# Kernel optimization log

Measured on AMD Instinct MI355X. Metric: run time of the kernel, lower is better.

Reference implementation:

```python
import jax, jax.numpy as jnp
import numpy as np

B, T, E, H = 2, 2048, 1024, 16
HS = E // H  # head size 64


def setup_inputs() -> dict:
    key = jax.random.key(0)
    ks = jax.random.split(key, 6)
    s = 0.02
    return {
        "x": jax.random.normal(ks[0], (B, T, E), dtype=jnp.float32),
        "Wq": jax.random.normal(ks[1], (E, E), dtype=jnp.float32) * s,
        "Wk": jax.random.normal(ks[2], (E, E), dtype=jnp.float32) * s,
        "Wv": jax.random.normal(ks[3], (E, E), dtype=jnp.float32) * s,
        "Wp": jax.random.normal(ks[4], (E, E), dtype=jnp.float32) * s,
        "bp": jax.random.normal(ks[5], (E,), dtype=jnp.float32) * s,
    }


def reference(x, Wq, Wk, Wv, Wp, bp):
    b, t, e = x.shape
    # per-head projections (concatenated heads == single E->E matmul, reshaped)
    def heads(w):
        return jnp.einsum('bte,ef->btf', x, w).reshape(b, t, H, HS).transpose(0, 2, 1, 3)
    q, k, v = heads(Wq), heads(Wk), heads(Wv)  # [B,H,T,HS]
    # NOTE: original scales by full embed dim E, not head_size
    scores = jnp.einsum('bhqd,bhkd->bhqk', q, k) * (e ** -0.5)
    causal = jnp.tril(jnp.ones((t, t), dtype=bool))
    scores = jnp.where(causal, scores, -jnp.inf)
    probs = jax.nn.softmax(scores, axis=-1)
    # dropout is identity in eval mode
    out = jnp.einsum('bhqk,bhkd->bhqd', probs, v)  # [B,H,T,HS]
    out = out.transpose(0, 2, 1, 3).reshape(b, t, e)
    return jnp.einsum('bte,ef->btf', out, Wp) + bp
```

## Files before the change

kernel.cpp:

```cpp
#include <hip/hip_runtime.h>
#include <math.h>

typedef __bf16 bf16x8 __attribute__((ext_vector_type(8)));
typedef __bf16 bf16x4 __attribute__((ext_vector_type(4)));
typedef float f32x4 __attribute__((ext_vector_type(4)));

constexpr int Bb = 2, Tt = 2048, Ee = 1024, Hh = 16, Hs = 64;
constexpr int Mm = Bb * Tt;

__device__ inline unsigned short f2bf(float f) {
    union { float f; unsigned u; } c; c.f = f;
    unsigned u = c.u;
    u += 0x7FFFu + ((u >> 16) & 1u);
    return (unsigned short)(u >> 16);
}

__device__ inline void gl2lds16(const void* g, void* l) {
    __builtin_amdgcn_global_load_lds(
        (const __attribute__((address_space(1))) void*)g,
        (__attribute__((address_space(3))) void*)l, 16, 0, 0);
}

__global__ __launch_bounds__(256) void prep(const float* __restrict__ x,
                                            const float* __restrict__ Wq,
                                            const float* __restrict__ Wk,
                                            const float* __restrict__ Wv,
                                            const float* __restrict__ Wp,
                                            unsigned short* __restrict__ xb,
                                            unsigned short* __restrict__ wt3,
                                            unsigned short* __restrict__ wpt) {
    const int tid = threadIdx.x;
    if (blockIdx.z == 4) {
        int flat = (blockIdx.y * 16 + blockIdx.x) * 256 + tid;
#pragma unroll
        for (int i = 0; i < 16; i++) {
            int gid = flat + i * 65536;
            float4 v = ((const float4*)x)[gid];
            ushort4 o;
            o.x = f2bf(v.x); o.y = f2bf(v.y); o.z = f2bf(v.z); o.w = f2bf(v.w);
            ((ushort4*)xb)[gid] = o;
        }
        return;
    }
    __shared__ unsigned short t[64][68];
    const float* W = (blockIdx.z == 0) ? Wq : (blockIdx.z == 1) ? Wk
                    : (blockIdx.z == 2) ? Wv : Wp;
    unsigned short* dst = (blockIdx.z < 3) ? wt3 + (size_t)blockIdx.z * 1024 * 1024 : wpt;
    const int k0 = blockIdx.x * 64, n0 = blockIdx.y * 64;
#pragma unroll
    for (int j = 0; j < 4; j++) {
        int row = (tid >> 4) + j * 16;
        int c4 = (tid & 15) * 4;
        float4 v = *(const float4*)&W[(size_t)(k0 + row) * 1024 + n0 + c4];
        t[row][c4 + 0] = f2bf(v.x); t[row][c4 + 1] = f2bf(v.y);
        t[row][c4 + 2] = f2bf(v.z); t[row][c4 + 3] = f2bf(v.w);
    }
    __syncthreads();
#pragma unroll
    for (int j = 0; j < 16; j++) {
        int flat = j * 256 + tid;
        int orow = flat >> 6, ocol = flat & 63;
        dst[(size_t)(n0 + orow) * 1024 + k0 + ocol] = t[ocol][orow];
    }
}

__device__ inline void gemm_mainloop(const unsigned short* __restrict__ A,
                                     const unsigned short* __restrict__ Bt,
                                     unsigned short* As, unsigned short* Bs,
                                     int bm, int bn, int tid, f32x4 (&acc)[4][4]) {
    const int lane = tid & 63, w = tid >> 6;
    const int quad = lane >> 4, cl = lane & 15;
    const int wm = (w >> 1) * 64, wn = (w & 1) * 64;

    auto stage = [&](int k0) {
#pragma unroll
        for (int i = 0; i < 2; i++) {
            int L = tid + i * 256;
            int r = L >> 2;
            int kc = (L & 3) ^ (r & 3);
            gl2lds16(A + (size_t)(bm + r) * 1024 + k0 + kc * 8, &As[L * 8]);
        }
#pragma unroll
        for (int i = 0; i < 2; i++) {
            int L = tid + i * 256;
            int r = L >> 2;
            int kc = (L & 3) ^ (r & 3);
            gl2lds16(Bt + (size_t)(bn + r) * 1024 + k0 + kc * 8, &Bs[L * 8]);
        }
    };

    stage(0);
    __syncthreads();
    for (int k0 = 0;;) {
        bf16x8 af[4], bfr[4];
#pragma unroll
        for (int mt = 0; mt < 4; mt++) {
            int r = wm + mt * 16 + cl;
            af[mt] = *(const bf16x8*)&As[(r * 4 + (quad ^ (r & 3))) * 8];
            int rb = wn + mt * 16 + cl;
            bfr[mt] = *(const bf16x8*)&Bs[(rb * 4 + (quad ^ (rb & 3))) * 8];
        }
#pragma unroll
        for (int mt = 0; mt < 4; mt++)
#pragma unroll
            for (int nt = 0; nt < 4; nt++)
                acc[mt][nt] = __builtin_amdgcn_mfma_f32_16x16x32_bf16(
                    af[mt], bfr[nt], acc[mt][nt], 0, 0, 0);
        k0 += 32;
        if (k0 >= 1024) break;
        __syncthreads();
        stage(k0);
        __syncthreads();
    }
}

__global__ __launch_bounds__(256, 2) void gemm_qkv(const unsigned short* __restrict__ A,
                                                   const unsigned short* __restrict__ Bt,
                                                   unsigned short* __restrict__ qb,
                                                   unsigned short* __restrict__ kb,
                                                   unsigned short* __restrict__ vtb) {
    __shared__ unsigned short As[128 * 32];
    __shared__ unsigned short Bs[128 * 32];
    const int tid = threadIdx.x;
    const int bm = blockIdx.y * 128;
    const int bn = blockIdx.x * 128;
    f32x4 acc[4][4] = {};
    gemm_mainloop(A, Bt, As, Bs, bm, bn, tid, acc);

    const int lane = tid & 63, w = tid >> 6;
    const int quad = lane >> 4, cl = lane & 15;
    const int wm = (w >> 1) * 64, wn = (w & 1) * 64;
    const int region = bn >> 10;

    if (region < 2) {
        unsigned short* dst = region ? kb : qb;
        const float qs = region ? 1.0f : 0.045084220027780107f;
#pragma unroll
        for (int mt = 0; mt < 4; mt++)
#pragma unroll
            for (int nt = 0; nt < 4; nt++)
#pragma unroll
                for (int rg = 0; rg < 4; rg++) {
                    int m = bm + wm + mt * 16 + quad * 4 + rg;
                    int nn = (bn + wn + nt * 16 + cl) & 1023;
                    int b = m >> 11, t = m & 2047, h = nn >> 6, hs = nn & 63;
                    dst[((size_t)(b * 16 + h) * 2048 + t) * 64 + hs] =
                        f2bf(acc[mt][nt][rg] * qs);
                }
    } else {
#pragma unroll
        for (int mt = 0; mt < 4; mt++) {
            int m0 = bm + wm + mt * 16 + quad * 4;
            int b = m0 >> 11, t0 = m0 & 2047;
#pragma unroll
            for (int nt = 0; nt < 4; nt++) {
                int nn = (bn + wn + nt * 16 + cl) & 1023;
                int h = nn >> 6, hs = nn & 63;
                ushort4 pk;
                pk.x = f2bf(acc[mt][nt][0]); pk.y = f2bf(acc[mt][nt][1]);
                pk.z = f2bf(acc[mt][nt][2]); pk.w = f2bf(acc[mt][nt][3]);
                *(ushort4*)&vtb[((size_t)(b * 16 + h) * 64 + hs) * 2048 + t0] = pk;
            }
        }
    }
}

__global__ __launch_bounds__(256, 4) void gemm_out(const unsigned short* __restrict__ A,
                                                   const unsigned short* __restrict__ Bt,
                                                   const float* __restrict__ bias,
                                                   float* __restrict__ out) {
    __shared__ unsigned short As[64 * 32];
    __shared__ unsigned short Bs[128 * 32];
    const int tid = threadIdx.x;
    const int bm = blockIdx.y * 64;
    const int bn = blockIdx.x * 128;
    const int lane = tid & 63, w = tid >> 6;
    const int quad = lane >> 4, cl = lane & 15;
    const int wm = (w >> 1) * 32, wn = (w & 1) * 64;
    f32x4 acc[2][4] = {};

    auto stage = [&](int k0) {
        {
            int L = tid;
            int r = L >> 2;
            int kc = (L & 3) ^ (r & 3);
            gl2lds16(A + (size_t)(bm + r) * 1024 + k0 + kc * 8, &As[L * 8]);
        }
#pragma unroll
        for (int i = 0; i < 2; i++) {
            int L = tid + i * 256;
            int r = L >> 2;
            int kc = (L & 3) ^ (r & 3);
            gl2lds16(Bt + (size_t)(bn + r) * 1024 + k0 + kc * 8, &Bs[L * 8]);
        }
    };

    stage(0);
    __syncthreads();
    for (int k0 = 0;;) {
        bf16x8 af[2], bfr[4];
#pragma unroll
        for (int mt = 0; mt < 2; mt++) {
            int r = wm + mt * 16 + cl;
            af[mt] = *(const bf16x8*)&As[(r * 4 + (quad ^ (r & 3))) * 8];
        }
#pragma unroll
        for (int nt = 0; nt < 4; nt++) {
            int rb = wn + nt * 16 + cl;
            bfr[nt] = *(const bf16x8*)&Bs[(rb * 4 + (quad ^ (rb & 3))) * 8];
        }
#pragma unroll
        for (int mt = 0; mt < 2; mt++)
#pragma unroll
            for (int nt = 0; nt < 4; nt++)
                acc[mt][nt] = __builtin_amdgcn_mfma_f32_16x16x32_bf16(
                    af[mt], bfr[nt], acc[mt][nt], 0, 0, 0);
        k0 += 32;
        if (k0 >= 1024) break;
        __syncthreads();
        stage(k0);
        __syncthreads();
    }

#pragma unroll
    for (int mt = 0; mt < 2; mt++)
#pragma unroll
        for (int nt = 0; nt < 4; nt++)
#pragma unroll
            for (int rg = 0; rg < 4; rg++) {
                int m = bm + wm + mt * 16 + quad * 4 + rg;
                int n = bn + wn + nt * 16 + cl;
                out[(size_t)m * 1024 + n] = acc[mt][nt][rg] + bias[n];
            }
}

__global__ __launch_bounds__(256, 3) void attn_mfma(const unsigned short* __restrict__ qg,
                                                    const unsigned short* __restrict__ kg,
                                                    const unsigned short* __restrict__ vtg,
                                                    unsigned short* __restrict__ og) {
    __shared__ unsigned short Qlds[128 * 64];
    __shared__ unsigned short Klds[2][64 * 64];
    __shared__ unsigned short Vlds[2][64 * 64];
    const int tid = threadIdx.x;
    const int idx = blockIdx.x;
    const int bh = idx & 31;
    const int j = 15 - (idx >> 5);
    const int lane = tid & 63, w = tid >> 6;
    const int quad = lane >> 4, cl = lane & 15;
    const int qbase = j * 128;
    const int wq0 = w * 32;
    const unsigned short* qB = qg + (size_t)bh * 2048 * 64;
    const unsigned short* kB = kg + (size_t)bh * 2048 * 64;
    const unsigned short* vB = vtg + (size_t)bh * 64 * 2048;

    auto stageKV = [&](int kt, int buf) {
#pragma unroll
        for (int i = 0; i < 2; i++) {
            int L = tid + i * 256;
            int r = L >> 3;
            int kc = (L & 7) ^ (r & 7);
            gl2lds16(kB + (size_t)(kt * 64 + r) * 64 + kc * 8, &Klds[buf][L * 8]);
            gl2lds16(vB + (size_t)r * 2048 + kt * 64 + kc * 8, &Vlds[buf][L * 8]);
        }
    };

#pragma unroll
    for (int i = 0; i < 4; i++) {
        int L = tid + i * 256;
        int r = L >> 3;
        int kc = (L & 7) ^ (r & 7);
        gl2lds16(qB + (size_t)(qbase + r) * 64 + kc * 8, &Qlds[L * 8]);
    }
    stageKV(0, 0);
    __syncthreads();

    bf16x8 qf[2][2];
#pragma unroll
    for (int nt2 = 0; nt2 < 2; nt2++)
#pragma unroll
        for (int kf = 0; kf < 2; kf++) {
            int r = wq0 + nt2 * 16 + cl, cc = kf * 4 + quad;
            qf[nt2][kf] = *(const bf16x8*)&Qlds[(r * 8 + (cc ^ (r & 7))) * 8];
        }

    bf16x8 ones;
#pragma unroll
    for (int i = 0; i < 8; i++) ones[i] = (__bf16)1.0f;

    f32x4 oacc[2][4] = {};
    f32x4 lacc[2] = {};
    unsigned short* Pw = &Qlds[w * 2048];
    const int ntiles = 2 * j + 2;
    const int dkt = 2 * j + (w >> 1);
    const int qloc0 = (w & 1) * 32;

    for (int kt = 0; kt < ntiles; kt++) {
        const int buf = kt & 1;
        if (kt + 1 < ntiles) stageKV(kt + 1, buf ^ 1);
        if (kt <= dkt) {
            const bool diag = (kt == dkt);
            f32x4 sac[4][2] = {};
#pragma unroll
            for (int kf = 0; kf < 2; kf++)
#pragma unroll
                for (int mt = 0; mt < 4; mt++) {
                    int r = mt * 16 + cl, cc = kf * 4 + quad;
                    bf16x8 kf8 = *(const bf16x8*)&Klds[buf][(r * 8 + (cc ^ (r & 7))) * 8];
#pragma unroll
                    for (int nt2 = 0; nt2 < 2; nt2++)
                        sac[mt][nt2] = __builtin_amdgcn_mfma_f32_16x16x32_bf16(
                            kf8, qf[nt2][kf], sac[mt][nt2], 0, 0, 0);
                }
#pragma unroll
            for (int mt = 0; mt < 4; mt++)
#pragma unroll
                for (int nt2 = 0; nt2 < 2; nt2++) {
                    bf16x4 p4;
#pragma unroll
                    for (int rg = 0; rg < 4; rg++) {
                        float p = exp2f(sac[mt][nt2][rg]);
                        if (diag && (mt * 16 + quad * 4 + rg > qloc0 + nt2 * 16 + cl))
                            p = 0.0f;
                        p4[rg] = (__bf16)p;
                    }
                    int r2 = nt2 * 16 + cl;
                    int c = mt * 2 + (quad >> 1);
                    *(bf16x4*)&Pw[(r2 * 8 + (c ^ (r2 & 7))) * 8 + (quad & 1) * 4] = p4;
                }
#pragma unroll
            for (int ks = 0; ks < 2; ks++) {
                bf16x8 pf[2];
#pragma unroll
                for (int mt2 = 0; mt2 < 2; mt2++) {
                    int r2 = mt2 * 16 + cl, cc = ks * 4 + quad;
                    pf[mt2] = *(const bf16x8*)&Pw[(r2 * 8 + (cc ^ (r2 & 7))) * 8];
                }
#pragma unroll
                for (int mt2 = 0; mt2 < 2; mt2++)
                    lacc[mt2] = __builtin_amdgcn_mfma_f32_16x16x32_bf16(
                        pf[mt2], ones, lacc[mt2], 0, 0, 0);
#pragma unroll
                for (int nt = 0; nt < 4; nt++) {
                    int r = nt * 16 + cl, cc = ks * 4 + quad;
                    bf16x8 vf = *(const bf16x8*)&Vlds[buf][(r * 8 + (cc ^ (r & 7))) * 8];
#pragma unroll
                    for (int mt2 = 0; mt2 < 2; mt2++)
                        oacc[mt2][nt] = __builtin_amdgcn_mfma_f32_16x16x32_bf16(
                            pf[mt2], vf, oacc[mt2][nt], 0, 0, 0);
                }
            }
        }
        __syncthreads();
    }

    const int b = bh >> 4, h = bh & 15;
#pragma unroll
    for (int mt2 = 0; mt2 < 2; mt2++)
#pragma unroll
        for (int rg = 0; rg < 4; rg++) {
            float inv = 1.0f / lacc[mt2][rg];
            int t = qbase + wq0 + mt2 * 16 + quad * 4 + rg;
#pragma unroll
            for (int nt = 0; nt < 4; nt++) {
                int hs = nt * 16 + cl;
                og[((size_t)(b * 2048 + t)) * 1024 + h * 64 + hs] =
                    f2bf(oacc[mt2][nt][rg] * inv);
            }
        }
}

extern "C" void kernel_launch(void* const* d_in, const int* in_sizes, int n_in,
                              void* d_out, int out_size, void* d_ws, size_t ws_size,
                              hipStream_t stream) {
    const float* x = (const float*)d_in[0];
    const float* Wq = (const float*)d_in[1];
    const float* Wk = (const float*)d_in[2];
    const float* Wv = (const float*)d_in[3];
    const float* Wp = (const float*)d_in[4];
    const float* bp = (const float*)d_in[5];
    float* out = (float*)d_out;

    unsigned short* xb = (unsigned short*)d_ws;
    unsigned short* wt3 = xb + (size_t)Mm * Ee;
    unsigned short* wpt = wt3 + (size_t)3 * Ee * Ee;
    unsigned short* qb = wpt + (size_t)Ee * Ee;
    unsigned short* kb = qb + (size_t)Mm * Ee;
    unsigned short* vtb = kb + (size_t)Mm * Ee;
    unsigned short* ab = vtb + (size_t)Mm * Ee;

    prep<<<dim3(16, 16, 5), dim3(256), 0, stream>>>(x, Wq, Wk, Wv, Wp, xb, wt3, wpt);
    gemm_qkv<<<dim3(24, 32), dim3(256), 0, stream>>>(xb, wt3, qb, kb, vtb);
    attn_mfma<<<dim3(512), dim3(256), 0, stream>>>(qb, kb, vtb, ab);
    gemm_out<<<dim3(8, 64), dim3(256), 0, stream>>>(ab, wpt, bp, out);
}
```

Baseline: 181.2 us.

## Split attention KV sequence across warp pairs with LDS combine and smaller query tiles

The attention kernel now uses 64-row query tiles, doubling the grid to 1024 blocks. The two warp pairs process alternating KV tiles in parallel (split-K within a block) and merge their partial output and row sums through LDS at the end. Q fragments are loaded straight from global memory instead of being staged in LDS. The aim is more blocks, better load balance over the causal triangle, and more parallelism per block. In exchange, KV staging is no longer double-buffered across iterations, so each iteration pays a load-then-sync stall, and there is an extra combine step.

Result: faster. 173.8 us (-4.1%).

```diff
diff --git a/kernel.cpp b/kernel.cpp
--- a/kernel.cpp
+++ b/kernel.cpp
@@ -238,49 +238,44 @@
                                                     const unsigned short* __restrict__ kg,
                                                     const unsigned short* __restrict__ vtg,
                                                     unsigned short* __restrict__ og) {
-    __shared__ unsigned short Qlds[128 * 64];
-    __shared__ unsigned short Klds[2][64 * 64];
-    __shared__ unsigned short Vlds[2][64 * 64];
+    __shared__ unsigned short lds[24576];
+    unsigned short* Plds = lds;
+    float* Cmb = (float*)(lds + 8192);
+    float* Ll  = (float*)(lds + 22528);
+
     const int tid = threadIdx.x;
     const int idx = blockIdx.x;
     const int bh = idx & 31;
-    const int j = 15 - (idx >> 5);
+    const int qt = 31 - (idx >> 5);
     const int lane = tid & 63, w = tid >> 6;
     const int quad = lane >> 4, cl = lane & 15;
-    const int qbase = j * 128;
-    const int wq0 = w * 32;
+    const int p = w >> 1;
+    const int qhalf = w & 1;
+    const int qbase = qt * 64;
     const unsigned short* qB = qg + (size_t)bh * 2048 * 64;
     const unsigned short* kB = kg + (size_t)bh * 2048 * 64;
     const unsigned short* vB = vtg + (size_t)bh * 64 * 2048;
 
     auto stageKV = [&](int kt, int buf) {
+        unsigned short* Kd = lds + 8192 + buf * 8192;
+        unsigned short* Vd = lds + 12288 + buf * 8192;
 #pragma unroll
         for (int i = 0; i < 2; i++) {
             int L = tid + i * 256;
             int r = L >> 3;
             int kc = (L & 7) ^ (r & 7);
-            gl2lds16(kB + (size_t)(kt * 64 + r) * 64 + kc * 8, &Klds[buf][L * 8]);
-            gl2lds16(vB + (size_t)r * 2048 + kt * 64 + kc * 8, &Vlds[buf][L * 8]);
+            gl2lds16(kB + (size_t)(kt * 64 + r) * 64 + kc * 8, &Kd[L * 8]);
+            gl2lds16(vB + (size_t)r * 2048 + kt * 64 + kc * 8, &Vd[L * 8]);
         }
     };
 
-#pragma unroll
-    for (int i = 0; i < 4; i++) {
-        int L = tid + i * 256;
-        int r = L >> 3;
-        int kc = (L & 7) ^ (r & 7);
-        gl2lds16(qB + (size_t)(qbase + r) * 64 + kc * 8, &Qlds[L * 8]);
-    }
-    stageKV(0, 0);
-    __syncthreads();
-
     bf16x8 qf[2][2];
 #pragma unroll
     for (int nt2 = 0; nt2 < 2; nt2++)
 #pragma unroll
         for (int kf = 0; kf < 2; kf++) {
-            int r = wq0 + nt2 * 16 + cl, cc = kf * 4 + quad;
-            qf[nt2][kf] = *(const bf16x8*)&Qlds[(r * 8 + (cc ^ (r & 7))) * 8];
+            int row = qbase + qhalf * 32 + nt2 * 16 + cl;
+            qf[nt2][kf] = *(const bf16x8*)&qB[(size_t)row * 64 + (kf * 4 + quad) * 8];
         }
 
     bf16x8 ones;
@@ -289,23 +284,26 @@
 
     f32x4 oacc[2][4] = {};
     f32x4 lacc[2] = {};
-    unsigned short* Pw = &Qlds[w * 2048];
-    const int ntiles = 2 * j + 2;
-    const int dkt = 2 * j + (w >> 1);
-    const int qloc0 = (w & 1) * 32;
-
-    for (int kt = 0; kt < ntiles; kt++) {
-        const int buf = kt & 1;
-        if (kt + 1 < ntiles) stageKV(kt + 1, buf ^ 1);
-        if (kt <= dkt) {
-            const bool diag = (kt == dkt);
+    unsigned short* Pw = &Plds[w * 2048];
+    const unsigned short* Kl = lds + 8192 + p * 8192;
+    const unsigned short* Vl = lds + 12288 + p * 8192;
+    const int nit = (qt + 2) >> 1;
+
+    for (int i = 0; i < nit; i++) {
+        stageKV(2 * i, 0);
+        if (2 * i + 1 <= qt) stageKV(2 * i + 1, 1);
+        __syncthreads();
+
+        const int kt = 2 * i + p;
+        if (kt <= qt) {
+            const bool diag = (kt == qt);
             f32x4 sac[4][2] = {};
 #pragma unroll
             for (int kf = 0; kf < 2; kf++)
 #pragma unroll
                 for (int mt = 0; mt < 4; mt++) {
                     int r = mt * 16 + cl, cc = kf * 4 + quad;
-                    bf16x8 kf8 = *(const bf16x8*)&Klds[buf][(r * 8 + (cc ^ (r & 7))) * 8];
+                    bf16x8 kf8 = *(const bf16x8*)&Kl[(r * 8 + (cc ^ (r & 7))) * 8];
 #pragma unroll
                     for (int nt2 = 0; nt2 < 2; nt2++)
                         sac[mt][nt2] = __builtin_amdgcn_mfma_f32_16x16x32_bf16(
@@ -318,10 +316,10 @@
                     bf16x4 p4;
 #pragma unroll
                     for (int rg = 0; rg < 4; rg++) {
-                        float p = exp2f(sac[mt][nt2][rg]);
-                        if (diag && (mt * 16 + quad * 4 + rg > qloc0 + nt2 * 16 + cl))
-                            p = 0.0f;
-                        p4[rg] = (__bf16)p;
+                        float pv = exp2f(sac[mt][nt2][rg]);
+                        if (diag && (mt * 16 + quad * 4 + rg > nt2 * 16 + cl + qhalf * 32))
+                            pv = 0.0f;
+                        p4[rg] = (__bf16)pv;
                     }
                     int r2 = nt2 * 16 + cl;
                     int c = mt * 2 + (quad >> 1);
@@ -342,7 +340,7 @@
 #pragma unroll
                 for (int nt = 0; nt < 4; nt++) {
                     int r = nt * 16 + cl, cc = ks * 4 + quad;
-                    bf16x8 vf = *(const bf16x8*)&Vlds[buf][(r * 8 + (cc ^ (r & 7))) * 8];
+                    bf16x8 vf = *(const bf16x8*)&Vl[(r * 8 + (cc ^ (r & 7))) * 8];
 #pragma unroll
                     for (int mt2 = 0; mt2 < 2; mt2++)
                         oacc[mt2][nt] = __builtin_amdgcn_mfma_f32_16x16x32_bf16(
@@ -353,20 +351,36 @@
         __syncthreads();
     }
 
-    const int b = bh >> 4, h = bh & 15;
-#pragma unroll
-    for (int mt2 = 0; mt2 < 2; mt2++)
-#pragma unroll
-        for (int rg = 0; rg < 4; rg++) {
-            float inv = 1.0f / lacc[mt2][rg];
-            int t = qbase + wq0 + mt2 * 16 + quad * 4 + rg;
-#pragma unroll
-            for (int nt = 0; nt < 4; nt++) {
-                int hs = nt * 16 + cl;
-                og[((size_t)(b * 2048 + t)) * 1024 + h * 64 + hs] =
-                    f2bf(oacc[mt2][nt][rg] * inv);
+    if (p == 1) {
+#pragma unroll
+        for (int mt2 = 0; mt2 < 2; mt2++)
+#pragma unroll
+            for (int rg = 0; rg < 4; rg++) {
+                int row = qhalf * 32 + mt2 * 16 + quad * 4 + rg;
+                if (cl == 0) Ll[row] = lacc[mt2][rg];
+#pragma unroll
+                for (int nt = 0; nt < 4; nt++)
+                    Cmb[row * 68 + nt * 16 + cl] = oacc[mt2][nt][rg];
             }
-        }
+    }
+    __syncthreads();
+    if (p == 0) {
+        const int b = bh >> 4, h = bh & 15;
+#pragma unroll
+        for (int mt2 = 0; mt2 < 2; mt2++)
+#pragma unroll
+            for (int rg = 0; rg < 4; rg++) {
+                int row = qhalf * 32 + mt2 * 16 + quad * 4 + rg;
+                float inv = 1.0f / (lacc[mt2][rg] + Ll[row]);
+                int t = qbase + row;
+#pragma unroll
+                for (int nt = 0; nt < 4; nt++) {
+                    int hs = nt * 16 + cl;
+                    float val = oacc[mt2][nt][rg] + Cmb[row * 68 + nt * 16 + cl];
+                    og[((size_t)(b * 2048 + t)) * 1024 + h * 64 + hs] = f2bf(val * inv);
+                }
+            }
+    }
 }
 
 extern "C" void kernel_launch(void* const* d_in, const int* in_sizes, int n_in,
@@ -390,6 +404,6 @@
 
     prep<<<dim3(16, 16, 5), dim3(256), 0, stream>>>(x, Wq, Wk, Wv, Wp, xb, wt3, wpt);
     gemm_qkv<<<dim3(24, 32), dim3(256), 0, stream>>>(xb, wt3, qb, kb, vtb);
-    attn_mfma<<<dim3(512), dim3(256), 0, stream>>>(qb, kb, vtb, ab);
+    attn_mfma<<<dim3(1024), dim3(256), 0, stream>>>(qb, kb, vtb, ab);
     gemm_out<<<dim3(8, 64), dim3(256), 0, stream>>>(ab, wpt, bp, out);
 }
```
